# Optimization experiments

Hardware: AMD Instinct MI355X
Metric: run time of the kernel (lower is better)

The kernel has to match this reference:

```python
import jax, jax.numpy as jnp
import numpy as np

N, E, C, R, HID = 50000, 500000, 64, 16, 64


def setup_inputs() -> dict:
    key = jax.random.key(0)
    ks = jax.random.split(key, 24)
    g = lambda k, shape, s=1.0: jax.random.normal(k, shape, dtype=jnp.float32) * s
    cs = C ** -0.5
    inp = {
        "h": g(ks[0], (N, 4 * C)),                                  # [N, 64x0e | 64x1o]
        "edge_index": jax.random.randint(ks[1], (2, E), 0, N),       # row0 = sender, row1 = receiver
        "edge_sh": g(ks[2], (E, 4)),                                 # Y_00, Y_1m (1x0e+1x1o)
        "edge_rbf": g(ks[3], (E, R)),                                # radial embedding 16x0e
        # interaction: linear_up (per-l channel mixing)
        "W_up0": g(ks[4], (C, C), cs), "W_up1": g(ks[5], (C, C), cs),
        # radial MLP 16->64->64->64->4*C (4 uvu tensor-product paths per channel)
        "M1": g(ks[6], (R, HID), R ** -0.5), "M2": g(ks[7], (HID, HID), HID ** -0.5),
        "M3": g(ks[8], (HID, HID), HID ** -0.5), "M4": g(ks[9], (HID, 4 * C), HID ** -0.5),
        # post-scatter linear
        "W_lin0": g(ks[10], (C, C), cs), "W_lin1": g(ks[11], (C, C), cs),
        # skip tensor product with 1x0e node attrs == linear residual
        "Wsc0": g(ks[12], (C, C), cs), "Wsc1": g(ks[13], (C, C), cs),
        # symmetric contraction weights (correlation <=3): 0e paths [a, a^2, v.v, a^3, a*v.v], 1o paths [v, a*v, a^2*v, (v.v)*v]
        "Wc0": g(ks[14], (C, 5)), "Wc1": g(ks[15], (C, 4)),
        # product-basis output linear
        "WB0": g(ks[16], (C, C), cs), "WB1": g(ks[17], (C, C), cs),
        # equivariant batchnorm affine params
        "gamma0": jnp.ones((C,), jnp.float32), "beta0": jnp.zeros((C,), jnp.float32),
        "gamma1": jnp.ones((C,), jnp.float32),
    }
    return inp


def reference(h, edge_index, edge_sh, edge_rbf, W_up0, W_up1, M1, M2, M3, M4,
              W_lin0, W_lin1, Wsc0, Wsc1, Wc0, Wc1, WB0, WB1, gamma0, beta0, gamma1):
    n = h.shape[0]
    h0 = h[:, :C]                        # [N,C] scalars
    h1 = h[:, C:].reshape(n, C, 3)       # [N,C,3] vectors

    # ---- interaction: linear_up ----
    up0 = h0 @ W_up0
    up1 = jnp.einsum('ncx,cd->ndx', h1, W_up1)

    # ---- radial MLP -> per-edge tensor-product weights [E,4,C] ----
    r = jax.nn.silu(edge_rbf @ M1)
    r = jax.nn.silu(r @ M2)
    r = jax.nn.silu(r @ M3)
    tpw = (r @ M4).reshape(-1, 4, C)

    # ---- gather + channelwise (uvu) tensor product with edge sh ----
    snd, rcv = edge_index[0], edge_index[1]
    x0 = up0[snd]                        # [E,C]
    x1 = up1[snd]                        # [E,C,3]
    sh0 = edge_sh[:, 0]                  # [E]
    sh1 = edge_sh[:, 1:]                 # [E,3]
    inv3 = 1.0 / jnp.sqrt(jnp.float32(3.0))
    # paths: 0e*0e->0e, 0e*1o->1o, 1o*0e->1o, 1o*1o->0e (dot)
    m0e = tpw[:, 0] * x0 * sh0[:, None] + tpw[:, 3] * jnp.einsum('ecx,ex->ec', x1, sh1) * inv3
    m1e = (tpw[:, 1][:, :, None] * x0[:, :, None] * sh1[:, None, :]
           + tpw[:, 2][:, :, None] * x1 * sh0[:, None, None])

    # ---- scatter-sum to receivers (avg_num_neighbors = 1.0) ----
    msg0 = jax.ops.segment_sum(m0e, rcv, num_segments=n)
    msg1 = jax.ops.segment_sum(m1e, rcv, num_segments=n)

    # ---- post linear -> A features; skip connection sc ----
    A0 = msg0 @ W_lin0
    A1 = jnp.einsum('ncx,cd->ndx', msg1, W_lin1)
    sc0 = h0 @ Wsc0
    sc1 = jnp.einsum('ncx,cd->ndx', h1, Wsc1)

    # ---- product basis: symmetric contraction up to correlation 3 ----
    vv = jnp.sum(A1 * A1, -1)            # [N,C]
    B0 = (Wc0[:, 0] * A0 + Wc0[:, 1] * A0 * A0 + Wc0[:, 2] * vv
          + Wc0[:, 3] * A0 ** 3 + Wc0[:, 4] * A0 * vv)
    B1 = (Wc1[:, 0] + Wc1[:, 1] * A0 + Wc1[:, 2] * A0 * A0 + Wc1[:, 3] * vv)[..., None] * A1
    o0 = B0 @ WB0 + sc0
    o1 = jnp.einsum('ncx,cd->ndx', B1, WB1) + sc1

    # ---- equivariant batchnorm: mean/var for 0e, norm-only for 1o ----
    eps = jnp.float32(1e-5)
    mu = jnp.mean(o0, 0)
    xc = o0 - mu
    var = jnp.mean(xc * xc, 0)
    n0 = xc * jax.lax.rsqrt(var + eps) * gamma0 + beta0
    nrm1 = jnp.mean(jnp.sum(o1 * o1, -1) / 3.0, 0)
    n1 = o1 * (jax.lax.rsqrt(nrm1 + eps) * gamma1)[None, :, None]

    return jnp.concatenate([n0, n1.reshape(n, 3 * C)], -1)
```

## Files before the change

### kernel.cpp

```cpp
#include <hip/hip_runtime.h>
#include <hip/hip_fp16.h>
#include <math.h>

#define NN 50000
#define NE 500000

typedef __attribute__((ext_vector_type(8))) short bf16x8;
typedef __attribute__((ext_vector_type(4))) float f32x4;

__device__ __forceinline__ float silu_f(float x) {
  return x / (1.0f + __expf(-x));
}
__device__ __forceinline__ unsigned short f2bf(float x) {
  union { float f; unsigned u; } v;
  v.f = x;
  unsigned r = v.u + 0x7fffu + ((v.u >> 16) & 1u);
  return (unsigned short)(r >> 16);
}
__device__ __forceinline__ unsigned short f2h(float x) {
  __half h = __float2half(x);
  return *reinterpret_cast<unsigned short*>(&h);
}
__device__ __forceinline__ float h2f(unsigned short u) {
  __half h = *reinterpret_cast<__half*>(&u);
  return __half2float(h);
}
__device__ __forceinline__ void splitbf(float x, unsigned short& hi_,
                                        unsigned short& lo_) {
  unsigned short h = f2bf(x);
  union { unsigned u; float f; } v;
  v.u = (unsigned)h << 16;
  hi_ = h;
  lo_ = f2bf(x - v.f);
}
__device__ __forceinline__ int swz64(int row, int col) {
  return row * 64 + ((((col >> 3) ^ (row & 7)) << 3) | (col & 7));
}
__device__ __forceinline__ int swz32(int row, int col) {
  return row * 32 + ((((col >> 3) ^ (row & 3)) << 3) | (col & 7));
}
__device__ __forceinline__ bf16x8 wfrag(const unsigned short* Wt, int n,
                                        int kc, int q) {
  return *reinterpret_cast<const bf16x8*>(
      &Wt[n * 64 + (((kc * 4 + q) ^ (n & 7)) << 3)]);
}
__device__ __forceinline__ bf16x8 ldfrag(const float* p) {
  float4 f0 = *reinterpret_cast<const float4*>(p);
  float4 f1 = *reinterpret_cast<const float4*>(p + 4);
  bf16x8 a;
  a[0] = (short)f2bf(f0.x); a[1] = (short)f2bf(f0.y);
  a[2] = (short)f2bf(f0.z); a[3] = (short)f2bf(f0.w);
  a[4] = (short)f2bf(f1.x); a[5] = (short)f2bf(f1.y);
  a[6] = (short)f2bf(f1.z); a[7] = (short)f2bf(f1.w);
  return a;
}
__device__ __forceinline__ void ldfrag2(const float* p, bf16x8& hi,
                                        bf16x8& lo) {
  float4 f0 = *reinterpret_cast<const float4*>(p);
  float4 f1 = *reinterpret_cast<const float4*>(p + 4);
  float a[8] = {f0.x, f0.y, f0.z, f0.w, f1.x, f1.y, f1.z, f1.w};
#pragma unroll
  for (int i = 0; i < 8; ++i) {
    unsigned short h, l2;
    splitbf(a[i], h, l2);
    hi[i] = (short)h;
    lo[i] = (short)l2;
  }
}
__device__ __forceinline__ f32x4 mfma_(bf16x8 a, bf16x8 b, f32x4 cacc) {
  return __builtin_amdgcn_mfma_f32_16x16x32_bf16(a, b, cacc, 0, 0, 0);
}

__global__ __launch_bounds__(256) void ksort1(const int* __restrict__ eidx,
                                              int* __restrict__ hist) {
  int e = blockIdx.x * 256 + threadIdx.x;
  if (e < NE) atomicAdd(&hist[eidx[NE + e]], 1);
}

__global__ __launch_bounds__(1024) void ksort2(const int* __restrict__ hist,
                                               int* __restrict__ cursor) {
  __shared__ int bs[1024];
  const int t = threadIdx.x;
  const int CH = (NN + 1023) / 1024;
  const int lo = t * CH, hi = (lo + CH < NN) ? lo + CH : NN;
  int s = 0;
  for (int i = lo; i < hi; ++i) s += hist[i];
  bs[t] = s;
  __syncthreads();
  for (int off = 1; off < 1024; off <<= 1) {
    int v = (t >= off) ? bs[t - off] : 0;
    __syncthreads();
    bs[t] += v;
    __syncthreads();
  }
  int run = bs[t] - s;
  for (int i = lo; i < hi; ++i) {
    cursor[i] = run;
    run += hist[i];
  }
}

#define EG_BLOCKS ((NE + 255) / 256)
__global__ __launch_bounds__(256) void ksort3_kup(
    const int* __restrict__ eidx, int* __restrict__ cursor,
    int* __restrict__ perm, const float* __restrict__ h,
    const float* __restrict__ Wup0, const float* __restrict__ Wup1,
    unsigned short* __restrict__ upb) {
  __shared__ float shd[4][256];
  if (blockIdx.x < EG_BLOCKS) {
    int e = blockIdx.x * 256 + threadIdx.x;
    if (e < NE) {
      int p = atomicAdd(&cursor[eidx[NE + e]], 1);
      perm[p] = e;
    }
    return;
  }
  const int w = threadIdx.x >> 6, j = threadIdx.x & 63;
  const int n = (blockIdx.x - EG_BLOCKS) * 4 + w;
  const float* hr = h + (size_t)n * 256;
#pragma unroll
  for (int t = 0; t < 4; ++t) shd[w][t * 64 + j] = hr[t * 64 + j];
  __syncthreads();
  float a0 = 0.f, ax = 0.f, ay = 0.f, az = 0.f;
#pragma unroll 8
  for (int c = 0; c < 64; ++c) {
    float h0 = shd[w][c];
    float hx = shd[w][64 + 3 * c + 0];
    float hy = shd[w][64 + 3 * c + 1];
    float hz = shd[w][64 + 3 * c + 2];
    float w0 = Wup0[c * 64 + j];
    float w1 = Wup1[c * 64 + j];
    a0 = fmaf(h0, w0, a0);
    ax = fmaf(hx, w1, ax);
    ay = fmaf(hy, w1, ay);
    az = fmaf(hz, w1, az);
  }
  ushort4 pk;
  pk.x = f2h(a0);
  pk.y = f2h(ax);
  pk.z = f2h(ay);
  pk.w = f2h(az);
  *reinterpret_cast<ushort4*>(upb + ((size_t)n * 64 + j) * 4) = pk;
}

__global__ __launch_bounds__(512) void kedge(
    const float* __restrict__ rbf, const int* __restrict__ eidx,
    const float* __restrict__ esh, const float* __restrict__ M1,
    const float* __restrict__ M2, const float* __restrict__ M3,
    const float* __restrict__ M4, const unsigned short* __restrict__ upb,
    const int* __restrict__ perm, float* __restrict__ msg0,
    float* __restrict__ msg1) {
  __shared__ unsigned short M1t[64 * 32];
  __shared__ unsigned short M2t[64 * 64];
  __shared__ unsigned short M3t[64 * 64];
  __shared__ unsigned short M4t[256 * 64];
  __shared__ unsigned short actS[8][32 * 64];
  const int tid = threadIdx.x;
  const int w = tid >> 6, l = tid & 63;
  const int c = l & 15, q = l >> 4;

  for (int i = tid; i < 2048; i += 512) {
    int o = i >> 5, k = i & 31;
    M1t[swz32(o, k)] = (k < 16) ? f2bf(M1[k * 64 + o]) : (unsigned short)0;
  }
  for (int i = tid; i < 4096; i += 512) {
    int k = i >> 6, o = i & 63;
    M2t[swz64(o, k)] = f2bf(M2[i]);
    M3t[swz64(o, k)] = f2bf(M3[i]);
  }
  for (int i = tid; i < 16384; i += 512) {
    int k = i >> 8, o = i & 255;
    M4t[swz64(o, k)] = f2bf(M4[i]);
  }
  __syncthreads();

  unsigned short* act = actS[w];
  const float inv3 = 0.57735026918962576f;
  const int NW = NE / 32;
  const int scq = (c >> 2) * 8 + (c & 3);

  for (int grp = blockIdx.x; grp < (NW + 7) / 8; grp += gridDim.x) {
    const int gw = grp * 8 + w;
    if (gw >= NW) continue;
    const int eb = gw * 32;

#pragma unroll
    for (int t = 0; t < 2; ++t) {
      const int sc = scq + t * 4;
      bf16x8 a1 = {};
      if (q < 2) {
        const int pec = perm[eb + sc];
        const float* p = rbf + (size_t)pec * 16 + q * 8;
        float4 f0 = *reinterpret_cast<const float4*>(p);
        float4 f1 = *reinterpret_cast<const float4*>(p + 4);
        a1[0] = (short)f2bf(f0.x); a1[1] = (short)f2bf(f0.y);
        a1[2] = (short)f2bf(f0.z); a1[3] = (short)f2bf(f0.w);
        a1[4] = (short)f2bf(f1.x); a1[5] = (short)f2bf(f1.y);
        a1[6] = (short)f2bf(f1.z); a1[7] = (short)f2bf(f1.w);
      }
      f32x4 acc[4];
#pragma unroll
      for (int nt = 0; nt < 4; ++nt) {
        int n = nt * 16 + c;
        bf16x8 b = *reinterpret_cast<const bf16x8*>(&M1t[n * 32 + ((q ^ (n & 3)) << 3)]);
        f32x4 z = {0.f, 0.f, 0.f, 0.f};
        acc[nt] = __builtin_amdgcn_mfma_f32_16x16x32_bf16(a1, b, z, 0, 0, 0);
      }
#pragma unroll
      for (int nt = 0; nt < 4; ++nt)
#pragma unroll
        for (int r = 0; r < 4; ++r)
          act[swz64(q * 8 + t * 4 + r, nt * 16 + c)] = f2bf(silu_f(acc[nt][r]));

      {
        bf16x8 a0 = *reinterpret_cast<const bf16x8*>(&act[sc * 64 + (((0 + q) ^ (sc & 7)) << 3)]);
        bf16x8 a1b = *reinterpret_cast<const bf16x8*>(&act[sc * 64 + (((4 + q) ^ (sc & 7)) << 3)]);
#pragma unroll
        for (int nt = 0; nt < 4; ++nt) {
          int n = nt * 16 + c;
          f32x4 z = {0.f, 0.f, 0.f, 0.f};
          acc[nt] = __builtin_amdgcn_mfma_f32_16x16x32_bf16(a0, wfrag(M2t, n, 0, q), z, 0, 0, 0);
          acc[nt] = __builtin_amdgcn_mfma_f32_16x16x32_bf16(a1b, wfrag(M2t, n, 1, q), acc[nt], 0, 0, 0);
        }
#pragma unroll
        for (int nt = 0; nt < 4; ++nt)
#pragma unroll
          for (int r = 0; r < 4; ++r)
            act[swz64(q * 8 + t * 4 + r, nt * 16 + c)] = f2bf(silu_f(acc[nt][r]));
      }
      {
        bf16x8 a0 = *reinterpret_cast<const bf16x8*>(&act[sc * 64 + (((0 + q) ^ (sc & 7)) << 3)]);
        bf16x8 a1b = *reinterpret_cast<const bf16x8*>(&act[sc * 64 + (((4 + q) ^ (sc & 7)) << 3)]);
#pragma unroll
        for (int nt = 0; nt < 4; ++nt) {
          int n = nt * 16 + c;
          f32x4 z = {0.f, 0.f, 0.f, 0.f};
          acc[nt] = __builtin_amdgcn_mfma_f32_16x16x32_bf16(a0, wfrag(M3t, n, 0, q), z, 0, 0, 0);
          acc[nt] = __builtin_amdgcn_mfma_f32_16x16x32_bf16(a1b, wfrag(M3t, n, 1, q), acc[nt], 0, 0, 0);
        }
#pragma unroll
        for (int nt = 0; nt < 4; ++nt)
#pragma unroll
          for (int r = 0; r < 4; ++r)
            act[swz64(q * 8 + t * 4 + r, nt * 16 + c)] = f2bf(silu_f(acc[nt][r]));
      }
    }

    int sn[8], rvv[8];
    float4 shv[8];
#pragma unroll
    for (int r8 = 0; r8 < 8; ++r8) {
      const int e2 = perm[eb + 8 * q + r8];
      sn[r8] = eidx[e2];
      rvv[r8] = eidx[NE + e2];
      shv[r8] = *reinterpret_cast<const float4*>(esh + (size_t)e2 * 4);
    }
    bf16x8 a0t[2], a1t[2];
#pragma unroll
    for (int t = 0; t < 2; ++t) {
      const int sc = scq + t * 4;
      a0t[t] = *reinterpret_cast<const bf16x8*>(&act[sc * 64 + (((0 + q) ^ (sc & 7)) << 3)]);
      a1t[t] = *reinterpret_cast<const bf16x8*>(&act[sc * 64 + (((4 + q) ^ (sc & 7)) << 3)]);
    }
#pragma unroll
    for (int j2 = 0; j2 < 4; ++j2) {
      const int ch = j2 * 16 + c;
      float acc0 = 0.f, accx = 0.f, accy = 0.f, accz = 0.f;
      int cur = rvv[0];
#pragma unroll
      for (int t = 0; t < 2; ++t) {
        ushort4 xv[4];
#pragma unroll
        for (int r = 0; r < 4; ++r)
          xv[r] = *reinterpret_cast<const ushort4*>(
              upb + ((size_t)sn[4 * t + r] * 64 + ch) * 4);
        f32x4 t4[4];
#pragma unroll
        for (int m = 0; m < 4; ++m) {
          int n = (m * 4 + j2) * 16 + c;
          f32x4 z = {0.f, 0.f, 0.f, 0.f};
          t4[m] = __builtin_amdgcn_mfma_f32_16x16x32_bf16(a0t[t], wfrag(M4t, n, 0, q), z, 0, 0, 0);
          t4[m] = __builtin_amdgcn_mfma_f32_16x16x32_bf16(a1t[t], wfrag(M4t, n, 1, q), t4[m], 0, 0, 0);
        }
#pragma unroll
        for (int r = 0; r < 4; ++r) {
          const int idx = 4 * t + r;
          float x0 = h2f(xv[r].x);
          float xx = h2f(xv[r].y);
          float xy = h2f(xv[r].z);
          float xz = h2f(xv[r].w);
          float t0v = t4[0][r], t1v = t4[1][r];
          float t2v = t4[2][r], t3v = t4[3][r];
          float4 sh4 = shv[idx];
          float dot = xx * sh4.y + xy * sh4.z + xz * sh4.w;
          float m0 = t0v * x0 * sh4.x + t3v * dot * inv3;
          float a1v = t1v * x0, b1v = t2v * sh4.x;
          float m1x = fmaf(a1v, sh4.y, b1v * xx);
          float m1y = fmaf(a1v, sh4.z, b1v * xy);
          float m1z = fmaf(a1v, sh4.w, b1v * xz);
          if (rvv[idx] != cur) {
            atomicAdd(msg0 + (size_t)cur * 64 + ch, acc0);
            atomicAdd(msg1 + (size_t)cur * 192 + ch, accx);
            atomicAdd(msg1 + (size_t)cur * 192 + 64 + ch, accy);
            atomicAdd(msg1 + (size_t)cur * 192 + 128 + ch, accz);
            cur = rvv[idx];
            acc0 = accx = accy = accz = 0.f;
          }
          acc0 += m0;
          accx += m1x;
          accy += m1y;
          accz += m1z;
        }
      }
      atomicAdd(msg0 + (size_t)cur * 64 + ch, acc0);
      atomicAdd(msg1 + (size_t)cur * 192 + ch, accx);
      atomicAdd(msg1 + (size_t)cur * 192 + 64 + ch, accy);
      atomicAdd(msg1 + (size_t)cur * 192 + 128 + ch, accz);
    }
  }
}

__global__ __launch_bounds__(512) void knode(
    const float* __restrict__ msg0, const float* __restrict__ msg1,
    const float* __restrict__ h, const float* __restrict__ Wl0,
    const float* __restrict__ Wl1, const float* __restrict__ Wsc0,
    const float* __restrict__ Wsc1, const float* __restrict__ Wc0,
    const float* __restrict__ Wc1, const float* __restrict__ WB0,
    const float* __restrict__ WB1, float* __restrict__ out,
    float* __restrict__ stat) {
  extern __shared__ unsigned short klds[];
  unsigned short* actS = klds + 10 * 4096;
  const int tid = threadIdx.x, w = tid >> 6, l = tid & 63;
  const int c = l & 15, q = l >> 4;
  for (int i = tid; i < 4096; i += 512) {
    int k = i >> 6, o = i & 63;
    int s = swz64(o, k);
    unsigned short hi, lo;
    splitbf(Wl0[i], hi, lo);
    klds[s] = hi; klds[4096 + s] = lo;
    splitbf(Wl1[i], hi, lo);
    klds[2 * 4096 + s] = hi; klds[3 * 4096 + s] = lo;
    klds[4 * 4096 + s] = f2bf(Wsc0[i]);
    klds[5 * 4096 + s] = f2bf(Wsc1[i]);
    splitbf(WB0[i], hi, lo);
    klds[6 * 4096 + s] = hi; klds[7 * 4096 + s] = lo;
    splitbf(WB1[i], hi, lo);
    klds[8 * 4096 + s] = hi; klds[9 * 4096 + s] = lo;
  }
  __syncthreads();
  const int gw = blockIdx.x * 8 + w;
  const bool valid = (gw < NN / 16);
  const int gws = valid ? gw : 0;
  const int n0 = gws * 16;
  const int nc = n0 + c;
  unsigned short* actH = actS + w * 2048;
  unsigned short* actL = actH + 1024;
  const unsigned short* Wl0h = klds;
  const unsigned short* Wl0l = klds + 4096;
  const unsigned short* Wl1h = klds + 2 * 4096;
  const unsigned short* Wl1l = klds + 3 * 4096;
  const unsigned short* Wsc0t = klds + 4 * 4096;
  const unsigned short* Wsc1t = klds + 5 * 4096;
  const unsigned short* WB0h = klds + 6 * 4096;
  const unsigned short* WB0l = klds + 7 * 4096;
  const unsigned short* WB1h = klds + 8 * 4096;
  const unsigned short* WB1l = klds + 9 * 4096;

  f32x4 aA0[4], aA1[3][4];
  {
    bf16x8 h0, l0, h1, l1;
    ldfrag2(msg0 + (size_t)nc * 64 + q * 8, h0, l0);
    ldfrag2(msg0 + (size_t)nc * 64 + 32 + q * 8, h1, l1);
#pragma unroll
    for (int nt = 0; nt < 4; ++nt) {
      int n = nt * 16 + c;
      f32x4 z = {0.f, 0.f, 0.f, 0.f};
      f32x4 v = mfma_(h0, wfrag(Wl0h, n, 0, q), z);
      v = mfma_(l0, wfrag(Wl0h, n, 0, q), v);
      v = mfma_(h0, wfrag(Wl0l, n, 0, q), v);
      v = mfma_(h1, wfrag(Wl0h, n, 1, q), v);
      v = mfma_(l1, wfrag(Wl0h, n, 1, q), v);
      v = mfma_(h1, wfrag(Wl0l, n, 1, q), v);
      aA0[nt] = v;
    }
#pragma unroll
    for (int x = 0; x < 3; ++x) {
      ldfrag2(msg1 + (size_t)nc * 192 + x * 64 + q * 8, h0, l0);
      ldfrag2(msg1 + (size_t)nc * 192 + x * 64 + 32 + q * 8, h1, l1);
#pragma unroll
      for (int nt = 0; nt < 4; ++nt) {
        int n = nt * 16 + c;
        f32x4 z = {0.f, 0.f, 0.f, 0.f};
        f32x4 v = mfma_(h0, wfrag(Wl1h, n, 0, q), z);
        v = mfma_(l0, wfrag(Wl1h, n, 0, q), v);
        v = mfma_(h0, wfrag(Wl1l, n, 0, q), v);
        v = mfma_(h1, wfrag(Wl1h, n, 1, q), v);
        v = mfma_(l1, wfrag(Wl1h, n, 1, q), v);
        v = mfma_(h1, wfrag(Wl1l, n, 1, q), v);
        aA1[x][nt] = v;
      }
    }
  }
#pragma unroll
  for (int nt = 0; nt < 4; ++nt) {
    const int ch = nt * 16 + c;
    const float* wc0 = Wc0 + ch * 5;
    const float4 c1 = *reinterpret_cast<const float4*>(Wc1 + ch * 4);
#pragma unroll
    for (int r = 0; r < 4; ++r) {
      float A0v = aA0[nt][r];
      float ax = aA1[0][nt][r], ay = aA1[1][nt][r], az = aA1[2][nt][r];
      float vv = ax * ax + ay * ay + az * az;
      float A02 = A0v * A0v;
      float B0 = wc0[0] * A0v + wc0[1] * A02 + wc0[2] * vv +
                 wc0[3] * A02 * A0v + wc0[4] * A0v * vv;
      float sB = c1.x + c1.y * A0v + c1.z * A02 + c1.w * vv;
      aA0[nt][r] = B0;
      aA1[0][nt][r] = sB * ax;
      aA1[1][nt][r] = sB * ay;
      aA1[2][nt][r] = sB * az;
    }
  }
  float st0[4], sq0[4], st1[4];
#pragma unroll
  for (int nt = 0; nt < 4; ++nt) { st0[nt] = 0.f; sq0[nt] = 0.f; st1[nt] = 0.f; }
  const float* hrow = h + (size_t)nc * 256;

  {
#pragma unroll
    for (int nt = 0; nt < 4; ++nt)
#pragma unroll
      for (int r = 0; r < 4; ++r) {
        unsigned short hh, ll;
        splitbf(aA0[nt][r], hh, ll);
        int s = swz64(4 * q + r, nt * 16 + c);
        actH[s] = hh;
        actL[s] = ll;
      }
    __syncthreads();
    bf16x8 bh0 = *reinterpret_cast<const bf16x8*>(&actH[c * 64 + ((q ^ (c & 7)) << 3)]);
    bf16x8 bh1 = *reinterpret_cast<const bf16x8*>(&actH[c * 64 + (((4 + q) ^ (c & 7)) << 3)]);
    bf16x8 bl0 = *reinterpret_cast<const bf16x8*>(&actL[c * 64 + ((q ^ (c & 7)) << 3)]);
    bf16x8 bl1 = *reinterpret_cast<const bf16x8*>(&actL[c * 64 + (((4 + q) ^ (c & 7)) << 3)]);
    __syncthreads();
    bf16x8 ah0 = ldfrag(hrow + q * 8);
    bf16x8 ah1 = ldfrag(hrow + 32 + q * 8);
    f32x4 o[4];
#pragma unroll
    for (int nt = 0; nt < 4; ++nt) {
      int n = nt * 16 + c;
      f32x4 z = {0.f, 0.f, 0.f, 0.f};
      f32x4 v = mfma_(ah0, wfrag(Wsc0t, n, 0, q), z);
      v = mfma_(ah1, wfrag(Wsc0t, n, 1, q), v);
      v = mfma_(bh0, wfrag(WB0h, n, 0, q), v);
      v = mfma_(bh1, wfrag(WB0h, n, 1, q), v);
      v = mfma_(bl0, wfrag(WB0h, n, 0, q), v);
      v = mfma_(bl1, wfrag(WB0h, n, 1, q), v);
      v = mfma_(bh0, wfrag(WB0l, n, 0, q), v);
      v = mfma_(bh1, wfrag(WB0l, n, 1, q), v);
      o[nt] = v;
    }
    if (valid) {
#pragma unroll
      for (int nt = 0; nt < 4; ++nt) {
        const int ch = nt * 16 + c;
#pragma unroll
        for (int r = 0; r < 4; ++r) {
          float v = o[nt][r];
          out[(size_t)(n0 + 4 * q + r) * 256 + ch] = v;
          st0[nt] += v;
          sq0[nt] = fmaf(v, v, sq0[nt]);
        }
      }
    }
  }
#pragma unroll
  for (int x = 0; x < 3; ++x) {
#pragma unroll
    for (int nt = 0; nt < 4; ++nt)
#pragma unroll
      for (int r = 0; r < 4; ++r) {
        unsigned short hh, ll;
        splitbf(aA1[x][nt][r], hh, ll);
        int s = swz64(4 * q + r, nt * 16 + c);
        actH[s] = hh;
        actL[s] = ll;
      }
    __syncthreads();
    bf16x8 bh0 = *reinterpret_cast<const bf16x8*>(&actH[c * 64 + ((q ^ (c & 7)) << 3)]);
    bf16x8 bh1 = *reinterpret_cast<const bf16x8*>(&actH[c * 64 + (((4 + q) ^ (c & 7)) << 3)]);
    bf16x8 bl0 = *reinterpret_cast<const bf16x8*>(&actL[c * 64 + ((q ^ (c & 7)) << 3)]);
    bf16x8 bl1 = *reinterpret_cast<const bf16x8*>(&actL[c * 64 + (((4 + q) ^ (c & 7)) << 3)]);
    __syncthreads();
    bf16x8 ah0, ah1;
#pragma unroll
    for (int i = 0; i < 8; ++i) {
      ah0[i] = (short)f2bf(hrow[64 + (q * 8 + i) * 3 + x]);
      ah1[i] = (short)f2bf(hrow[64 + (32 + q * 8 + i) * 3 + x]);
    }
    f32x4 o[4];
#pragma unroll
    for (int nt = 0; nt < 4; ++nt) {
      int n = nt * 16 + c;
      f32x4 z = {0.f, 0.f, 0.f, 0.f};
      f32x4 v = mfma_(ah0, wfrag(Wsc1t, n, 0, q), z);
      v = mfma_(ah1, wfrag(Wsc1t, n, 1, q), v);
      v = mfma_(bh0, wfrag(WB1h, n, 0, q), v);
      v = mfma_(bh1, wfrag(WB1h, n, 1, q), v);
      v = mfma_(bl0, wfrag(WB1h, n, 0, q), v);
      v = mfma_(bl1, wfrag(WB1h, n, 1, q), v);
      v = mfma_(bh0, wfrag(WB1l, n, 0, q), v);
      v = mfma_(bh1, wfrag(WB1l, n, 1, q), v);
      o[nt] = v;
    }
    if (valid) {
#pragma unroll
      for (int nt = 0; nt < 4; ++nt) {
        const int ch = nt * 16 + c;
#pragma unroll
        for (int r = 0; r < 4; ++r) {
          float v = o[nt][r];
          out[(size_t)(n0 + 4 * q + r) * 256 + 64 + 3 * ch + x] = v;
          st1[nt] = fmaf(v, v, st1[nt]);
        }
      }
    }
  }
  if (valid) {
#pragma unroll
    for (int nt = 0; nt < 4; ++nt) {
      float v0 = st0[nt], v1 = sq0[nt], v2 = st1[nt];
      v0 += __shfl_xor(v0, 16); v0 += __shfl_xor(v0, 32);
      v1 += __shfl_xor(v1, 16); v1 += __shfl_xor(v1, 32);
      v2 += __shfl_xor(v2, 16); v2 += __shfl_xor(v2, 32);
      if (q == 0) {
        atomicAdd(stat + nt * 16 + c, v0);
        atomicAdd(stat + 64 + nt * 16 + c, v1);
        atomicAdd(stat + 128 + nt * 16 + c, v2);
      }
    }
  }
}

__global__ void kstat(const float* __restrict__ stat_in,
                      float* __restrict__ stat_out,
                      const float* __restrict__ gamma0,
                      const float* __restrict__ gamma1) {
  const int j = threadIdx.x;
  const float invN = 1.0f / (float)NN;
  float mu = stat_in[j] * invN;
  float var = stat_in[64 + j] * invN - mu * mu;
  float s0 = rsqrtf(var + 1e-5f) * gamma0[j];
  float nr = stat_in[128 + j] * (invN / 3.0f);
  float s1 = rsqrtf(nr + 1e-5f) * gamma1[j];
  stat_out[j] = mu;
  stat_out[64 + j] = s0;
  stat_out[128 + j] = s1;
}

__global__ __launch_bounds__(256) void knorm(float* __restrict__ out,
                                             const float* __restrict__ stat,
                                             const float* __restrict__ beta0) {
  const int w = threadIdx.x >> 6, j = threadIdx.x & 63;
  const int n = blockIdx.x * 4 + w;
  const float mu = stat[192 + j], s0 = stat[256 + j], s1 = stat[320 + j];
  const float b0 = beta0[j];
  float* orow = out + (size_t)n * 256;
  orow[j] = (orow[j] - mu) * s0 + b0;
#pragma unroll
  for (int x = 0; x < 3; ++x) orow[64 + 3 * j + x] *= s1;
}

extern "C" void kernel_launch(void* const* d_in, const int* in_sizes, int n_in,
                              void* d_out, int out_size, void* d_ws,
                              size_t ws_size, hipStream_t stream) {
  (void)in_sizes; (void)n_in; (void)out_size; (void)ws_size;
  const float* h = (const float*)d_in[0];
  const int* eidx = (const int*)d_in[1];
  const float* esh = (const float*)d_in[2];
  const float* erbf = (const float*)d_in[3];
  const float* Wup0 = (const float*)d_in[4];
  const float* Wup1 = (const float*)d_in[5];
  const float* M1 = (const float*)d_in[6];
  const float* M2 = (const float*)d_in[7];
  const float* M3 = (const float*)d_in[8];
  const float* M4 = (const float*)d_in[9];
  const float* Wl0 = (const float*)d_in[10];
  const float* Wl1 = (const float*)d_in[11];
  const float* Wsc0 = (const float*)d_in[12];
  const float* Wsc1 = (const float*)d_in[13];
  const float* Wc0 = (const float*)d_in[14];
  const float* Wc1 = (const float*)d_in[15];
  const float* WB0 = (const float*)d_in[16];
  const float* WB1 = (const float*)d_in[17];
  const float* gamma0 = (const float*)d_in[18];
  const float* beta0 = (const float*)d_in[19];
  const float* gamma1 = (const float*)d_in[20];

  float* ws = (float*)d_ws;
  unsigned short* upb = (unsigned short*)ws;
  float* msg0 = ws + (size_t)NN * 256;
  float* msg1 = ws + (size_t)NN * 320;
  float* stat = ws + (size_t)NN * 512;
  float* outf = (float*)d_out;

  int* hist = (int*)d_out;
  int* cursor = hist + NN;
  int* perm = cursor + NN;

  hipMemsetAsync(msg0, 0, ((size_t)NN * 256 + 384) * sizeof(float), stream);
  hipMemsetAsync(hist, 0, (size_t)NN * sizeof(int), stream);

  hipFuncSetAttribute((const void*)knode,
                      hipFuncAttributeMaxDynamicSharedMemorySize, 114688);

  ksort1<<<EG_BLOCKS, 256, 0, stream>>>(eidx, hist);
  ksort2<<<1, 1024, 0, stream>>>(hist, cursor);
  ksort3_kup<<<EG_BLOCKS + NN / 4, 256, 0, stream>>>(eidx, cursor, perm, h,
                                                     Wup0, Wup1, upb);
  kedge<<<512, 512, 0, stream>>>(erbf, eidx, esh, M1, M2, M3, M4, upb, perm,
                                 msg0, msg1);
  knode<<<(NN / 16 + 7) / 8, 512, 114688, stream>>>(
      msg0, msg1, h, Wl0, Wl1, Wsc0, Wsc1, Wc0, Wc1, WB0, WB1, outf, stat);
  kstat<<<1, 64, 0, stream>>>(stat, stat + 192, gamma0, gamma1);
  knorm<<<NN / 4, 256, 0, stream>>>(outf, stat, beta0);
}
```

Measured before the change: 484.0 us.

## Move low-part and skip weights to global prepped buffer, shrink knode LDS, fold kstat

The fp32 weights are still split into hi/lo bf16 halves, but now the lo halves and the single-bf16 skip weights are swizzled once by extra blocks appended to the histogram kernel and stored in a global buffer. knode keeps only the four hi tiles in LDS (64KB instead of 112KB), aiming for more resident blocks per CU and less per-block setup. The kstat kernel is removed and its mean/scale math is recomputed inside knorm, saving one launch. In exchange, MFMA B-fragments for the lo and skip tiles are now read from global memory through cache instead of LDS, and knorm redoes the rsqrt work in every thread.

```diff
diff --git a/kernel.cpp b/kernel.cpp
--- a/kernel.cpp
+++ b/kernel.cpp
@@ -4,6 +4,7 @@
 
 #define NN 50000
 #define NE 500000
+#define EG_BLOCKS ((NE + 255) / 256)
 
 typedef __attribute__((ext_vector_type(8))) short bf16x8;
 typedef __attribute__((ext_vector_type(4))) float f32x4;
@@ -71,10 +72,31 @@
   return __builtin_amdgcn_mfma_f32_16x16x32_bf16(a, b, cacc, 0, 0, 0);
 }
 
-__global__ __launch_bounds__(256) void ksort1(const int* __restrict__ eidx,
-                                              int* __restrict__ hist) {
-  int e = blockIdx.x * 256 + threadIdx.x;
-  if (e < NE) atomicAdd(&hist[eidx[NE + e]], 1);
+__global__ __launch_bounds__(256) void ksort1_prep(
+    const int* __restrict__ eidx, int* __restrict__ hist,
+    const float* __restrict__ Wl0, const float* __restrict__ Wl1,
+    const float* __restrict__ WB0, const float* __restrict__ WB1,
+    const float* __restrict__ Wsc0, const float* __restrict__ Wsc1,
+    unsigned short* __restrict__ wswz) {
+  if (blockIdx.x < EG_BLOCKS) {
+    int e = blockIdx.x * 256 + threadIdx.x;
+    if (e < NE) atomicAdd(&hist[eidx[NE + e]], 1);
+    return;
+  }
+  const int idx = (blockIdx.x - EG_BLOCKS) * 256 + threadIdx.x;
+  const int tile = idx >> 12, i = idx & 4095;
+  const int k = i >> 6, o = i & 63;
+  const int s = swz64(o, k);
+  unsigned short hi, lo, v;
+  switch (tile) {
+    case 0: splitbf(Wl0[i], hi, lo); v = lo; break;
+    case 1: splitbf(Wl1[i], hi, lo); v = lo; break;
+    case 2: splitbf(WB0[i], hi, lo); v = lo; break;
+    case 3: splitbf(WB1[i], hi, lo); v = lo; break;
+    case 4: v = f2bf(Wsc0[i]); break;
+    default: v = f2bf(Wsc1[i]); break;
+  }
+  wswz[tile * 4096 + s] = v;
 }
 
 __global__ __launch_bounds__(1024) void ksort2(const int* __restrict__ hist,
@@ -100,7 +122,6 @@
   }
 }
 
-#define EG_BLOCKS ((NE + 255) / 256)
 __global__ __launch_bounds__(256) void ksort3_kup(
     const int* __restrict__ eidx, int* __restrict__ cursor,
     int* __restrict__ perm, const float* __restrict__ h,
@@ -323,29 +344,21 @@
 __global__ __launch_bounds__(512) void knode(
     const float* __restrict__ msg0, const float* __restrict__ msg1,
     const float* __restrict__ h, const float* __restrict__ Wl0,
-    const float* __restrict__ Wl1, const float* __restrict__ Wsc0,
-    const float* __restrict__ Wsc1, const float* __restrict__ Wc0,
-    const float* __restrict__ Wc1, const float* __restrict__ WB0,
-    const float* __restrict__ WB1, float* __restrict__ out,
-    float* __restrict__ stat) {
+    const float* __restrict__ Wl1, const float* __restrict__ WB0,
+    const float* __restrict__ WB1, const float* __restrict__ Wc0,
+    const float* __restrict__ Wc1, const unsigned short* __restrict__ wswz,
+    float* __restrict__ out, float* __restrict__ stat) {
   extern __shared__ unsigned short klds[];
-  unsigned short* actS = klds + 10 * 4096;
+  unsigned short* actS = klds + 4 * 4096;
   const int tid = threadIdx.x, w = tid >> 6, l = tid & 63;
   const int c = l & 15, q = l >> 4;
   for (int i = tid; i < 4096; i += 512) {
     int k = i >> 6, o = i & 63;
     int s = swz64(o, k);
-    unsigned short hi, lo;
-    splitbf(Wl0[i], hi, lo);
-    klds[s] = hi; klds[4096 + s] = lo;
-    splitbf(Wl1[i], hi, lo);
-    klds[2 * 4096 + s] = hi; klds[3 * 4096 + s] = lo;
-    klds[4 * 4096 + s] = f2bf(Wsc0[i]);
-    klds[5 * 4096 + s] = f2bf(Wsc1[i]);
-    splitbf(WB0[i], hi, lo);
-    klds[6 * 4096 + s] = hi; klds[7 * 4096 + s] = lo;
-    splitbf(WB1[i], hi, lo);
-    klds[8 * 4096 + s] = hi; klds[9 * 4096 + s] = lo;
+    klds[s] = f2bf(Wl0[i]);
+    klds[4096 + s] = f2bf(Wl1[i]);
+    klds[2 * 4096 + s] = f2bf(WB0[i]);
+    klds[3 * 4096 + s] = f2bf(WB1[i]);
   }
   __syncthreads();
   const int gw = blockIdx.x * 8 + w;
@@ -356,15 +369,15 @@
   unsigned short* actH = actS + w * 2048;
   unsigned short* actL = actH + 1024;
   const unsigned short* Wl0h = klds;
-  const unsigned short* Wl0l = klds + 4096;
-  const unsigned short* Wl1h = klds + 2 * 4096;
-  const unsigned short* Wl1l = klds + 3 * 4096;
-  const unsigned short* Wsc0t = klds + 4 * 4096;
-  const unsigned short* Wsc1t = klds + 5 * 4096;
-  const unsigned short* WB0h = klds + 6 * 4096;
-  const unsigned short* WB0l = klds + 7 * 4096;
-  const unsigned short* WB1h = klds + 8 * 4096;
-  const unsigned short* WB1l = klds + 9 * 4096;
+  const unsigned short* Wl1h = klds + 4096;
+  const unsigned short* WB0h = klds + 2 * 4096;
+  const unsigned short* WB1h = klds + 3 * 4096;
+  const unsigned short* Wl0l = wswz;
+  const unsigned short* Wl1l = wswz + 4096;
+  const unsigned short* WB0l = wswz + 2 * 4096;
+  const unsigned short* WB1l = wswz + 3 * 4096;
+  const unsigned short* Wsc0t = wswz + 4 * 4096;
+  const unsigned short* Wsc1t = wswz + 5 * 4096;
 
   f32x4 aA0[4], aA1[3][4];
   {
@@ -542,28 +555,19 @@
   }
 }
 
-__global__ void kstat(const float* __restrict__ stat_in,
-                      float* __restrict__ stat_out,
-                      const float* __restrict__ gamma0,
-                      const float* __restrict__ gamma1) {
-  const int j = threadIdx.x;
-  const float invN = 1.0f / (float)NN;
-  float mu = stat_in[j] * invN;
-  float var = stat_in[64 + j] * invN - mu * mu;
-  float s0 = rsqrtf(var + 1e-5f) * gamma0[j];
-  float nr = stat_in[128 + j] * (invN / 3.0f);
-  float s1 = rsqrtf(nr + 1e-5f) * gamma1[j];
-  stat_out[j] = mu;
-  stat_out[64 + j] = s0;
-  stat_out[128 + j] = s1;
-}
-
 __global__ __launch_bounds__(256) void knorm(float* __restrict__ out,
                                              const float* __restrict__ stat,
+                                             const float* __restrict__ gamma0,
+                                             const float* __restrict__ gamma1,
                                              const float* __restrict__ beta0) {
   const int w = threadIdx.x >> 6, j = threadIdx.x & 63;
   const int n = blockIdx.x * 4 + w;
-  const float mu = stat[192 + j], s0 = stat[256 + j], s1 = stat[320 + j];
+  const float invN = 1.0f / (float)NN;
+  const float mu = stat[j] * invN;
+  const float var = stat[64 + j] * invN - mu * mu;
+  const float s0 = rsqrtf(var + 1e-5f) * gamma0[j];
+  const float nr = stat[128 + j] * (invN / 3.0f);
+  const float s1 = rsqrtf(nr + 1e-5f) * gamma1[j];
   const float b0 = beta0[j];
   float* orow = out + (size_t)n * 256;
   orow[j] = (orow[j] - mu) * s0 + b0;
@@ -602,6 +606,8 @@
   float* msg0 = ws + (size_t)NN * 256;
   float* msg1 = ws + (size_t)NN * 320;
   float* stat = ws + (size_t)NN * 512;
+  unsigned short* wswz =
+      (unsigned short*)(ws + (size_t)NN * 512 + 384);
   float* outf = (float*)d_out;
 
   int* hist = (int*)d_out;
@@ -612,16 +618,17 @@
   hipMemsetAsync(hist, 0, (size_t)NN * sizeof(int), stream);
 
   hipFuncSetAttribute((const void*)knode,
-                      hipFuncAttributeMaxDynamicSharedMemorySize, 114688);
-
-  ksort1<<<EG_BLOCKS, 256, 0, stream>>>(eidx, hist);
+                      hipFuncAttributeMaxDynamicSharedMemorySize, 65536);
+
+  ksort1_prep<<<EG_BLOCKS + 96, 256, 0, stream>>>(eidx, hist, Wl0, Wl1, WB0,
+                                                  WB1, Wsc0, Wsc1, wswz);
   ksort2<<<1, 1024, 0, stream>>>(hist, cursor);
   ksort3_kup<<<EG_BLOCKS + NN / 4, 256, 0, stream>>>(eidx, cursor, perm, h,
                                                      Wup0, Wup1, upb);
   kedge<<<512, 512, 0, stream>>>(erbf, eidx, esh, M1, M2, M3, M4, upb, perm,
                                  msg0, msg1);
-  knode<<<(NN / 16 + 7) / 8, 512, 114688, stream>>>(
-      msg0, msg1, h, Wl0, Wl1, Wsc0, Wsc1, Wc0, Wc1, WB0, WB1, outf, stat);
-  kstat<<<1, 64, 0, stream>>>(stat, stat + 192, gamma0, gamma1);
-  knorm<<<NN / 4, 256, 0, stream>>>(outf, stat, beta0);
-}
+  knode<<<(NN / 16 + 7) / 8, 512, 65536, stream>>>(msg0, msg1, h, Wl0, Wl1,
+                                                   WB0, WB1, Wc0, Wc1, wswz,
+                                                   outf, stat);
+  knorm<<<NN / 4, 256, 0, stream>>>(outf, stat, gamma0, gamma1, beta0);
+}
```

New measurement: 490.1 us. About the same (+1.3%).
